# Optimization experiments

Measured on AMD Instinct MI355X. Metric: run time of the kernel, lower is better.

Reference implementation:

```python
import jax, jax.numpy as jnp
import numpy as np

S, B, D, H = 2048, 2, 1024, 16
DK = D // H
SCALE = 1.0 / np.sqrt(DK)


def setup_inputs() -> dict:
    key = jax.random.key(0)
    ks = jax.random.split(key, 8)
    return {
        "query": jax.random.normal(ks[0], (S, B, D), dtype=jnp.float32),
        "key": jax.random.normal(ks[1], (S, B, D), dtype=jnp.float32),
        "value": jax.random.normal(ks[2], (S, B, D), dtype=jnp.float32),
        "mask": jax.random.randint(ks[3], (B, S, S), 0, 2, dtype=jnp.int32),
        "in_proj_weight": jax.random.normal(ks[4], (3 * D, D), dtype=jnp.float32) * 0.02,
        "in_proj_bias": jax.random.normal(ks[5], (3 * D,), dtype=jnp.float32) * 0.02,
        "out_proj_weight": jax.random.normal(ks[6], (D, D), dtype=jnp.float32) * 0.02,
        "out_proj_bias": jax.random.normal(ks[7], (D,), dtype=jnp.float32) * 0.02,
    }


def reference(query, key, value, mask, in_proj_weight, in_proj_bias,
              out_proj_weight, out_proj_bias):
    seq_len, batch, d_model = query.shape
    # split fused in-projection: order is query, key, value
    Wq, Wk, Wv = in_proj_weight[:D], in_proj_weight[D:2 * D], in_proj_weight[2 * D:]
    bq, bk, bv = in_proj_bias[:D], in_proj_bias[D:2 * D], in_proj_bias[2 * D:]
    # PrepareForMultiHeadAttention: x @ W^T + b, then split heads -> [s, b, h, d_k]
    q = (query @ Wq.T + bq).reshape(seq_len, batch, H, DK)
    k = (key @ Wk.T + bk).reshape(key.shape[0], batch, H, DK)
    v = (value @ Wv.T + bv).reshape(value.shape[0], batch, H, DK)
    # scores [i, j, b, h] in float32, scaled
    scores = jnp.einsum('ibhd,jbhd->ijbh', q, k).astype(jnp.float32) * SCALE
    # mask: [b, q, k] -> permute(1,2,0) -> [q, k, b] -> unsqueeze(-1)
    m = jnp.transpose(mask, (1, 2, 0))[..., None]
    scores = jnp.where(m == 1, jnp.float32(-1e9), scores)
    # softmax over key axis (dim=1)
    attn = jax.nn.softmax(scores, axis=1)
    # dropout p=0.0 -> identity
    x = jnp.einsum('ijbh,jbhd->ibhd', attn, v).reshape(seq_len, batch, -1)
    return x @ out_proj_weight.T + out_proj_bias
```

## Files before the change

kernel.cpp:

```cpp
#include <hip/hip_runtime.h>
#include <hip/hip_bf16.h>

typedef unsigned short u16;
typedef unsigned int   u32;
typedef unsigned long long u64;
typedef __bf16 bf16x8 __attribute__((ext_vector_type(8)));
typedef float  f32x4  __attribute__((ext_vector_type(4)));

#define S_LEN  2048
#define BATCH  2
#define DMODEL 1024
#define NHEADS 16
#define DKH    64
#define MWORDS (S_LEN/64)
#define ATT_SCALE 0.125f

__device__ __forceinline__ u16 f2bf(float f){
  u32 x = __builtin_bit_cast(u32, f);
  x += 0x7fffu + ((x >> 16) & 1u);
  return (u16)(x >> 16);
}
__device__ __forceinline__ bf16x8 ld8(const u16* p){ return *(const bf16x8*)p; }

__device__ __forceinline__ void gload16(const u16* g, u16* l){
  __builtin_amdgcn_global_load_lds(
      (const __attribute__((address_space(1))) u32*)(u64)g,
      (__attribute__((address_space(3))) u32*)(u64)l,
      16, 0, 0);
}

__global__ __launch_bounds__(256) void cvt_kernel(
    const float* __restrict__ a0, const float* __restrict__ a1, const float* __restrict__ a2,
    const float* __restrict__ wi, const float* __restrict__ wo, const int* __restrict__ msk,
    u16* __restrict__ d0, u16* __restrict__ d1, u16* __restrict__ d2,
    u16* __restrict__ dwi, u16* __restrict__ dwo, u64* __restrict__ mbits)
{
  int tid = blockIdx.x*256 + threadIdx.x;
  int stride = gridDim.x*256;
  const int NX = S_LEN*BATCH*DMODEL/4;
  for (int i = tid; i < NX; i += stride){
    f32x4 x0 = ((const f32x4*)a0)[i];
    f32x4 x1 = ((const f32x4*)a1)[i];
    f32x4 x2 = ((const f32x4*)a2)[i];
    ((ushort4*)d0)[i] = make_ushort4(f2bf(x0[0]), f2bf(x0[1]), f2bf(x0[2]), f2bf(x0[3]));
    ((ushort4*)d1)[i] = make_ushort4(f2bf(x1[0]), f2bf(x1[1]), f2bf(x1[2]), f2bf(x1[3]));
    ((ushort4*)d2)[i] = make_ushort4(f2bf(x2[0]), f2bf(x2[1]), f2bf(x2[2]), f2bf(x2[3]));
  }
  const int NWI = 3*DMODEL*DMODEL/4;
  for (int i = tid; i < NWI; i += stride){
    f32x4 x = ((const f32x4*)wi)[i];
    ((ushort4*)dwi)[i] = make_ushort4(f2bf(x[0]), f2bf(x[1]), f2bf(x[2]), f2bf(x[3]));
  }
  const int NWO = DMODEL*DMODEL/4;
  for (int i = tid; i < NWO; i += stride){
    f32x4 x = ((const f32x4*)wo)[i];
    ((ushort4*)dwo)[i] = make_ushort4(f2bf(x[0]), f2bf(x[1]), f2bf(x[2]), f2bf(x[3]));
  }
  int gw   = tid >> 6;
  int lane = threadIdx.x & 63;
  int nwaves = stride >> 6;
  const int NW = BATCH*S_LEN*MWORDS;
  for (int w4 = gw*4; w4 < NW; w4 += nwaves*4){
    int v0 = msk[(size_t)(w4+0)*64 + lane];
    int v1 = msk[(size_t)(w4+1)*64 + lane];
    int v2 = msk[(size_t)(w4+2)*64 + lane];
    int v3 = msk[(size_t)(w4+3)*64 + lane];
    u64 b0 = __ballot(v0 != 0);
    u64 b1 = __ballot(v1 != 0);
    u64 b2 = __ballot(v2 != 0);
    u64 b3 = __ballot(v3 != 0);
    if (lane == 0){
      mbits[w4+0] = b0; mbits[w4+1] = b1;
      mbits[w4+2] = b2; mbits[w4+3] = b3;
    }
  }
}

__device__ __forceinline__ void gemm128_loop(
    const u16* __restrict__ A, const u16* __restrict__ W,
    u16* abuf, u16* bbuf, int tid, f32x4 acc[4][4])
{
  int lane = tid & 63, quad = lane >> 4, r = lane & 15;
  int wv = tid >> 6, wm = (wv & 1)*64, wn = (wv >> 1)*64;
  int c0 = tid, c1 = tid + 256;
  int r0 = c0 >> 2, g0 = ((c0 & 3) ^ (r0 & 3))*8;
  int r1 = c1 >> 2, g1 = ((c1 & 3) ^ (r1 & 3))*8;
  const u16* ga0 = A + (size_t)r0*DMODEL + g0;
  const u16* ga1 = A + (size_t)r1*DMODEL + g1;
  const u16* gb0 = W + (size_t)r0*DMODEL + g0;
  const u16* gb1 = W + (size_t)r1*DMODEL + g1;
  int sw = (quad ^ (r & 3))*8;

  auto stage = [&](int bu, int k0){
    u16* ab = abuf + bu*(128*32);
    u16* bb = bbuf + bu*(128*32);
    gload16(ga0 + k0, ab + c0*8);
    gload16(ga1 + k0, ab + c1*8);
    gload16(gb0 + k0, bb + c0*8);
    gload16(gb1 + k0, bb + c1*8);
  };
  auto step = [&](int bu){
    const u16* ab = abuf + bu*(128*32);
    const u16* bb = bbuf + bu*(128*32);
    bf16x8 af[4], bfr[4];
    #pragma unroll
    for (int i = 0; i < 4; ++i) af[i]  = ld8(&ab[(wm + i*16 + r)*32 + sw]);
    #pragma unroll
    for (int i = 0; i < 4; ++i) bfr[i] = ld8(&bb[(wn + i*16 + r)*32 + sw]);
    #pragma unroll
    for (int mi = 0; mi < 4; ++mi)
      #pragma unroll
      for (int ni = 0; ni < 4; ++ni)
        acc[mi][ni] = __builtin_amdgcn_mfma_f32_16x16x32_bf16(af[mi], bfr[ni], acc[mi][ni], 0,0,0);
  };

  stage(0, 0);
  __syncthreads();
  for (int k0 = 0; k0 < DMODEL; k0 += 64){
    stage(1, k0 + 32);
    step(0);
    __syncthreads();
    if (k0 + 64 < DMODEL) stage(0, k0 + 64);
    step(1);
    __syncthreads();
  }
}

__global__ __launch_bounds__(256) void qkv_proj_kernel(
    const u16* __restrict__ xq, const u16* __restrict__ xk, const u16* __restrict__ xv,
    const u16* __restrict__ w, const float* __restrict__ bias,
    u16* __restrict__ q_ws, u16* __restrict__ k_ws, u16* __restrict__ vt_ws)
{
  __shared__ __align__(16) u16 abuf[2*128*32];
  __shared__ __align__(16) u16 bbuf[2*128*32];
  int tid = threadIdx.x;
  int lane = tid & 63, quad = lane >> 4, r = lane & 15;
  int wv = tid >> 6, wm = (wv & 1)*64, wn = (wv >> 1)*64;
  int m0 = blockIdx.x*128, n0 = blockIdx.y*128;
  int t = n0 >> 10;
  const u16* X = (t == 0) ? xq : (t == 1) ? xk : xv;

  f32x4 acc[4][4] = {};
  gemm128_loop(X + (size_t)m0*DMODEL, w + (size_t)n0*DMODEL, abuf, bbuf, tid, acc);

  int mbase = m0 + wm, nbase = n0 + wn;
  #pragma unroll
  for (int ni = 0; ni < 4; ++ni){
    int n  = nbase + ni*16 + r;
    float bv = bias[n];
    int nn = n & (DMODEL-1);
    int h = nn >> 6, dk = nn & 63;
    #pragma unroll
    for (int mi = 0; mi < 4; ++mi){
      #pragma unroll
      for (int reg = 0; reg < 4; ++reg){
        int m = mbase + mi*16 + quad*4 + reg;
        int s = m >> 1, b = m & 1;
        u16 hv = f2bf(acc[mi][ni][reg] + bv);
        size_t bh = (size_t)(b*NHEADS + h);
        if (t == 0)      q_ws [(bh*S_LEN + s)*DKH + dk] = hv;
        else if (t == 1) k_ws [(bh*S_LEN + s)*DKH + dk] = hv;
        else             vt_ws[(bh*DKH + dk)*S_LEN + s] = hv;
      }
    }
  }
}

__global__ __launch_bounds__(256) void attn_kernel(
    const u16* __restrict__ q_ws, const u16* __restrict__ k_ws, const u16* __restrict__ vt_ws,
    const u64* __restrict__ mbits, u16* __restrict__ x_ws)
{
  __shared__ __align__(16) u16 kbuf[2][64*72];
  __shared__ __align__(16) u16 vbuf[2][64*72];
  __shared__ __align__(16) u16 pbuf[4][16*72];
  int tid  = threadIdx.x;
  int wv   = tid >> 6;
  int lane = tid & 63;
  int quad = lane >> 4, r = lane & 15;

  int lin  = blockIdx.y * 32 + blockIdx.x;
  int xcd  = lin & 7, slot = lin >> 3;
  int bh   = (xcd << 2) | (slot >> 5);
  int xt   = slot & 31;
  int b  = bh >> 4, h = bh & 15;
  int i0 = (xt*4 + wv) * 16;

  const u16* Q  = q_ws  + (size_t)bh*S_LEN*DKH;
  const u16* K  = k_ws  + (size_t)bh*S_LEN*DKH;
  const u16* Vt = vt_ws + (size_t)bh*DKH*S_LEN;
  const u64* MB = mbits + ((size_t)b*S_LEN + (i0 + r))*MWORDS;

  int f1 = tid + 256;
  int sr0 = tid >> 3, sc0 = (tid & 7)*8;
  int sr1 = f1  >> 3, sc1 = (f1  & 7)*8;

  const u16* qrow = Q + (size_t)(i0 + r)*DKH + quad*8;
  bf16x8 qf0 = ld8(qrow), qf1 = ld8(qrow + 32);

  float l_part = 0.f;
  f32x4 o[4] = {};
  f32x4 z = {0.f, 0.f, 0.f, 0.f};
  u16* pl = pbuf[wv];

  bf16x8 ak0, ak1, av0, av1, bk0, bk1, bv0, bv1;

  auto loadset = [&](bf16x8& kv0, bf16x8& kv1, bf16x8& vv0, bf16x8& vv1, int j0){
    kv0 = ld8(K  + (size_t)(j0 + sr0)*DKH + sc0);
    kv1 = ld8(K  + (size_t)(j0 + sr1)*DKH + sc1);
    vv0 = ld8(Vt + (size_t)sr0*S_LEN + j0 + sc0);
    vv1 = ld8(Vt + (size_t)sr1*S_LEN + j0 + sc1);
  };
  auto storeset = [&](u16* kb, u16* vb, bf16x8 kv0, bf16x8 kv1, bf16x8 vv0, bf16x8 vv1){
    *(bf16x8*)&kb[sr0*72 + sc0] = kv0;
    *(bf16x8*)&kb[sr1*72 + sc1] = kv1;
    *(bf16x8*)&vb[sr0*72 + sc0] = vv0;
    *(bf16x8*)&vb[sr1*72 + sc1] = vv1;
  };
  auto compute = [&](const u16* kb, const u16* vb, u64 mb){
    float p[16];
    #pragma unroll
    for (int c = 0; c < 4; ++c){
      bf16x8 ka = ld8(&kb[(16*c + r)*72 + quad*8]);
      bf16x8 k8 = ld8(&kb[(16*c + r)*72 + 32 + quad*8]);
      __builtin_amdgcn_s_setprio(1);
      f32x4 s = __builtin_amdgcn_mfma_f32_16x16x32_bf16(ka, qf0, z, 0,0,0);
      s       = __builtin_amdgcn_mfma_f32_16x16x32_bf16(k8, qf1, s, 0,0,0);
      __builtin_amdgcn_s_setprio(0);
      u32 mc = (u32)(mb >> (16*c + 4*quad));
      p[c*4+0] = (mc & 1u) ? 0.f : __expf(s[0]*ATT_SCALE);
      p[c*4+1] = (mc & 2u) ? 0.f : __expf(s[1]*ATT_SCALE);
      p[c*4+2] = (mc & 4u) ? 0.f : __expf(s[2]*ATT_SCALE);
      p[c*4+3] = (mc & 8u) ? 0.f : __expf(s[3]*ATT_SCALE);
      l_part += p[c*4+0] + p[c*4+1] + p[c*4+2] + p[c*4+3];
    }
    #pragma unroll
    for (int c = 0; c < 4; ++c)
      *(ushort4*)&pl[r*72 + 16*c + quad*4] =
        make_ushort4(f2bf(p[c*4+0]), f2bf(p[c*4+1]), f2bf(p[c*4+2]), f2bf(p[c*4+3]));
    asm volatile("s_waitcnt lgkmcnt(0)" ::: "memory");
    bf16x8 pf0 = ld8(&pl[r*72 + quad*8]);
    bf16x8 pf1 = ld8(&pl[r*72 + 32 + quad*8]);
    __builtin_amdgcn_s_setprio(1);
    #pragma unroll
    for (int tt = 0; tt < 4; ++tt){
      bf16x8 va = ld8(&vb[(tt*16 + r)*72 + quad*8]);
      bf16x8 v8 = ld8(&vb[(tt*16 + r)*72 + 32 + quad*8]);
      o[tt] = __builtin_amdgcn_mfma_f32_16x16x32_bf16(pf0, va, o[tt], 0,0,0);
      o[tt] = __builtin_amdgcn_mfma_f32_16x16x32_bf16(pf1, v8, o[tt], 0,0,0);
    }
    __builtin_amdgcn_s_setprio(0);
  };

  loadset(ak0, ak1, av0, av1, 0);
  storeset(kbuf[0], vbuf[0], ak0, ak1, av0, av1);
  loadset(bk0, bk1, bv0, bv1, 64);
  __syncthreads();

  for (int j0 = 0; j0 < S_LEN; j0 += 128){
    storeset(kbuf[1], vbuf[1], bk0, bk1, bv0, bv1);
    if (j0 + 128 < S_LEN) loadset(ak0, ak1, av0, av1, j0 + 128);
    compute(kbuf[0], vbuf[0], MB[j0 >> 6]);
    __syncthreads();
    if (j0 + 128 < S_LEN) storeset(kbuf[0], vbuf[0], ak0, ak1, av0, av1);
    if (j0 + 192 < S_LEN) loadset(bk0, bk1, bv0, bv1, j0 + 192);
    compute(kbuf[1], vbuf[1], MB[(j0 >> 6) + 1]);
    __syncthreads();
  }

  l_part += __shfl_xor(l_part, 16, 64);
  l_part += __shfl_xor(l_part, 32, 64);
  float l0 = 1.f/__shfl(l_part, quad*4+0, 64);
  float l1 = 1.f/__shfl(l_part, quad*4+1, 64);
  float l2 = 1.f/__shfl(l_part, quad*4+2, 64);
  float l3 = 1.f/__shfl(l_part, quad*4+3, 64);
  #pragma unroll
  for (int tt = 0; tt < 4; ++tt){
    int col = h*DKH + tt*16 + r;
    x_ws[((size_t)(i0 + quad*4 + 0)*BATCH + b)*DMODEL + col] = f2bf(o[tt][0]*l0);
    x_ws[((size_t)(i0 + quad*4 + 1)*BATCH + b)*DMODEL + col] = f2bf(o[tt][1]*l1);
    x_ws[((size_t)(i0 + quad*4 + 2)*BATCH + b)*DMODEL + col] = f2bf(o[tt][2]*l2);
    x_ws[((size_t)(i0 + quad*4 + 3)*BATCH + b)*DMODEL + col] = f2bf(o[tt][3]*l3);
  }
}

__global__ __launch_bounds__(256) void out_proj_kernel(
    const u16* __restrict__ x, const u16* __restrict__ w, const float* __restrict__ bias,
    float* __restrict__ out)
{
  __shared__ __align__(16) u16 abuf[2*128*32];
  __shared__ __align__(16) u16 bbuf[2*128*32];
  int tid = threadIdx.x;
  int lane = tid & 63, quad = lane >> 4, r = lane & 15;
  int wv = tid >> 6, wm = (wv & 1)*64, wn = (wv >> 1)*64;
  int m0 = blockIdx.x*128, n0 = blockIdx.y*128;

  f32x4 acc[4][4] = {};
  gemm128_loop(x + (size_t)m0*DMODEL, w + (size_t)n0*DMODEL, abuf, bbuf, tid, acc);

  int mbase = m0 + wm, nbase = n0 + wn;
  #pragma unroll
  for (int ni = 0; ni < 4; ++ni){
    int n = nbase + ni*16 + r;
    float bv = bias[n];
    #pragma unroll
    for (int mi = 0; mi < 4; ++mi){
      #pragma unroll
      for (int reg = 0; reg < 4; ++reg){
        int m = mbase + mi*16 + quad*4 + reg;
        out[(size_t)m*DMODEL + n] = acc[mi][ni][reg] + bv;
      }
    }
  }
}

extern "C" void kernel_launch(void* const* d_in, const int* in_sizes, int n_in,
                              void* d_out, int out_size, void* d_ws, size_t ws_size,
                              hipStream_t stream) {
  (void)in_sizes; (void)n_in; (void)out_size; (void)ws_size;
  const float* query = (const float*)d_in[0];
  const float* key   = (const float*)d_in[1];
  const float* value = (const float*)d_in[2];
  const int*   mask  = (const int*)d_in[3];
  const float* w_in  = (const float*)d_in[4];
  const float* b_in  = (const float*)d_in[5];
  const float* w_out = (const float*)d_in[6];
  const float* b_out = (const float*)d_in[7];
  float* out = (float*)d_out;

  const size_t TSZ = (size_t)BATCH*NHEADS*S_LEN*DKH;
  const size_t XSZ = (size_t)S_LEN*BATCH*DMODEL;
  u16* q_ws  = (u16*)d_ws;
  u16* k_ws  = q_ws  + TSZ;
  u16* vt_ws = k_ws  + TSZ;
  u16* x_ws  = vt_ws + TSZ;
  u16* xq_bf = x_ws  + XSZ;
  u16* xk_bf = xq_bf + XSZ;
  u16* xv_bf = xk_bf + XSZ;
  u16* wi_bf = xv_bf + XSZ;
  u16* wo_bf = wi_bf + (size_t)3*DMODEL*DMODEL;
  u64* mb_ws = (u64*)(wo_bf + (size_t)DMODEL*DMODEL);

  cvt_kernel<<<1024, 256, 0, stream>>>(query, key, value, w_in, w_out, mask,
                                       xq_bf, xk_bf, xv_bf, wi_bf, wo_bf, mb_ws);
  qkv_proj_kernel<<<dim3(32, 24), 256, 0, stream>>>(xq_bf, xk_bf, xv_bf, wi_bf, b_in,
                                                    q_ws, k_ws, vt_ws);
  attn_kernel<<<dim3(32, 32), 256, 0, stream>>>(q_ws, k_ws, vt_ws, mb_ws, x_ws);
  out_proj_kernel<<<dim3(32, 8), 256, 0, stream>>>(x_ws, wo_bf, b_out, out);
}
```

Before: 289.0 us.

## Double attention block to 8 waves with XOR-swizzled LDS tiles and packed bf16 convert

The attention kernel now uses 512-thread blocks of 8 waves covering 128 query rows, so each K/V tile staged in LDS is shared by twice as many waves and per-thread global loads are halved. The padded 72-stride LDS layout is replaced by a 64-stride XOR swizzle for the K, V and P buffers to avoid bank conflicts without padding. The P conversion uses the packed v_cvt_pk_bf16_f32 instruction. The trade-offs are fewer blocks in the grid, more threads waiting at each barrier, and more swizzle index arithmetic.

New measurement: 251.2 us. 13.1% less time.

```diff
diff --git a/kernel.cpp b/kernel.cpp
--- a/kernel.cpp
+++ b/kernel.cpp
@@ -21,6 +21,12 @@
   return (u16)(x >> 16);
 }
 __device__ __forceinline__ bf16x8 ld8(const u16* p){ return *(const bf16x8*)p; }
+
+__device__ __forceinline__ u32 pk_bf16(float a, float b){
+  u32 d;
+  asm("v_cvt_pk_bf16_f32 %0, %1, %2" : "=v"(d) : "v"(a), "v"(b));
+  return d;
+}
 
 __device__ __forceinline__ void gload16(const u16* g, u16* l){
   __builtin_amdgcn_global_load_lds(
@@ -166,62 +172,67 @@
   }
 }
 
-__global__ __launch_bounds__(256) void attn_kernel(
+__global__ __launch_bounds__(512) void attn_kernel(
     const u16* __restrict__ q_ws, const u16* __restrict__ k_ws, const u16* __restrict__ vt_ws,
     const u64* __restrict__ mbits, u16* __restrict__ x_ws)
 {
-  __shared__ __align__(16) u16 kbuf[2][64*72];
-  __shared__ __align__(16) u16 vbuf[2][64*72];
-  __shared__ __align__(16) u16 pbuf[4][16*72];
+  __shared__ __align__(16) u16 kbuf[2][64*64];
+  __shared__ __align__(16) u16 vbuf[2][64*64];
+  __shared__ __align__(16) u16 pbuf[8][16*64];
   int tid  = threadIdx.x;
   int wv   = tid >> 6;
   int lane = tid & 63;
   int quad = lane >> 4, r = lane & 15;
 
-  int lin  = blockIdx.y * 32 + blockIdx.x;
+  int lin  = blockIdx.y * 16 + blockIdx.x;
   int xcd  = lin & 7, slot = lin >> 3;
-  int bh   = (xcd << 2) | (slot >> 5);
-  int xt   = slot & 31;
+  int bh   = (xcd << 2) | (slot >> 4);
+  int xt   = slot & 15;
   int b  = bh >> 4, h = bh & 15;
-  int i0 = (xt*4 + wv) * 16;
+  int i0 = (xt*8 + wv) * 16;
 
   const u16* Q  = q_ws  + (size_t)bh*S_LEN*DKH;
   const u16* K  = k_ws  + (size_t)bh*S_LEN*DKH;
   const u16* Vt = vt_ws + (size_t)bh*DKH*S_LEN;
   const u64* MB = mbits + ((size_t)b*S_LEN + (i0 + r))*MWORDS;
 
-  int f1 = tid + 256;
-  int sr0 = tid >> 3, sc0 = (tid & 7)*8;
-  int sr1 = f1  >> 3, sc1 = (f1  & 7)*8;
+  int sr  = tid >> 3;
+  int sc8 = (tid & 7) * 8;
+  int ssw = ((tid & 7) ^ (sr & 7)) * 8;
+  const u16* Kp = K  + (size_t)sr*DKH   + sc8;
+  const u16* Vp = Vt + (size_t)sr*S_LEN + sc8;
 
   const u16* qrow = Q + (size_t)(i0 + r)*DKH + quad*8;
   bf16x8 qf0 = ld8(qrow), qf1 = ld8(qrow + 32);
+
+  int m7   = r & 7;
+  int ksw0 = (quad ^ m7) * 8;
+  int ksw1 = ksw0 ^ 32;
+  int pw0  = ((quad >> 1) ^ m7) * 8 + (quad & 1)*4;
 
   float l_part = 0.f;
   f32x4 o[4] = {};
   f32x4 z = {0.f, 0.f, 0.f, 0.f};
   u16* pl = pbuf[wv];
 
-  bf16x8 ak0, ak1, av0, av1, bk0, bk1, bv0, bv1;
-
-  auto loadset = [&](bf16x8& kv0, bf16x8& kv1, bf16x8& vv0, bf16x8& vv1, int j0){
-    kv0 = ld8(K  + (size_t)(j0 + sr0)*DKH + sc0);
-    kv1 = ld8(K  + (size_t)(j0 + sr1)*DKH + sc1);
-    vv0 = ld8(Vt + (size_t)sr0*S_LEN + j0 + sc0);
-    vv1 = ld8(Vt + (size_t)sr1*S_LEN + j0 + sc1);
-  };
-  auto storeset = [&](u16* kb, u16* vb, bf16x8 kv0, bf16x8 kv1, bf16x8 vv0, bf16x8 vv1){
-    *(bf16x8*)&kb[sr0*72 + sc0] = kv0;
-    *(bf16x8*)&kb[sr1*72 + sc1] = kv1;
-    *(bf16x8*)&vb[sr0*72 + sc0] = vv0;
-    *(bf16x8*)&vb[sr1*72 + sc1] = vv1;
-  };
-  auto compute = [&](const u16* kb, const u16* vb, u64 mb){
+  bf16x8 ka_, va_, kb_, vb_;
+  auto loadset = [&](bf16x8& kv, bf16x8& vv, int j0){
+    kv = ld8(Kp + (size_t)j0*DKH);
+    vv = ld8(Vp + j0);
+  };
+  auto storeset = [&](int bu, bf16x8 kv, bf16x8 vv){
+    *(bf16x8*)&kbuf[bu][sr*64 + ssw] = kv;
+    *(bf16x8*)&vbuf[bu][sr*64 + ssw] = vv;
+  };
+  auto compute = [&](int bu, u64 mb){
+    const u16* kb = kbuf[bu];
+    const u16* vb = vbuf[bu];
     float p[16];
     #pragma unroll
     for (int c = 0; c < 4; ++c){
-      bf16x8 ka = ld8(&kb[(16*c + r)*72 + quad*8]);
-      bf16x8 k8 = ld8(&kb[(16*c + r)*72 + 32 + quad*8]);
+      int rowb = (16*c + r)*64;
+      bf16x8 ka = ld8(&kb[rowb + ksw0]);
+      bf16x8 k8 = ld8(&kb[rowb + ksw1]);
       __builtin_amdgcn_s_setprio(1);
       f32x4 s = __builtin_amdgcn_mfma_f32_16x16x32_bf16(ka, qf0, z, 0,0,0);
       s       = __builtin_amdgcn_mfma_f32_16x16x32_bf16(k8, qf1, s, 0,0,0);
@@ -234,36 +245,39 @@
       l_part += p[c*4+0] + p[c*4+1] + p[c*4+2] + p[c*4+3];
     }
     #pragma unroll
-    for (int c = 0; c < 4; ++c)
-      *(ushort4*)&pl[r*72 + 16*c + quad*4] =
-        make_ushort4(f2bf(p[c*4+0]), f2bf(p[c*4+1]), f2bf(p[c*4+2]), f2bf(p[c*4+3]));
+    for (int c = 0; c < 4; ++c){
+      u32 k0 = pk_bf16(p[c*4+0], p[c*4+1]);
+      u32 k1 = pk_bf16(p[c*4+2], p[c*4+3]);
+      *(uint2*)&pl[r*64 + ((pw0 & ~7) ^ (2*c*8)) + (pw0 & 7)] = make_uint2(k0, k1);
+    }
     asm volatile("s_waitcnt lgkmcnt(0)" ::: "memory");
-    bf16x8 pf0 = ld8(&pl[r*72 + quad*8]);
-    bf16x8 pf1 = ld8(&pl[r*72 + 32 + quad*8]);
+    bf16x8 pf0 = ld8(&pl[r*64 + ksw0]);
+    bf16x8 pf1 = ld8(&pl[r*64 + ksw1]);
     __builtin_amdgcn_s_setprio(1);
     #pragma unroll
     for (int tt = 0; tt < 4; ++tt){
-      bf16x8 va = ld8(&vb[(tt*16 + r)*72 + quad*8]);
-      bf16x8 v8 = ld8(&vb[(tt*16 + r)*72 + 32 + quad*8]);
+      int rowb = (tt*16 + r)*64;
+      bf16x8 va = ld8(&vb[rowb + ksw0]);
+      bf16x8 v8 = ld8(&vb[rowb + ksw1]);
       o[tt] = __builtin_amdgcn_mfma_f32_16x16x32_bf16(pf0, va, o[tt], 0,0,0);
       o[tt] = __builtin_amdgcn_mfma_f32_16x16x32_bf16(pf1, v8, o[tt], 0,0,0);
     }
     __builtin_amdgcn_s_setprio(0);
   };
 
-  loadset(ak0, ak1, av0, av1, 0);
-  storeset(kbuf[0], vbuf[0], ak0, ak1, av0, av1);
-  loadset(bk0, bk1, bv0, bv1, 64);
+  loadset(ka_, va_, 0);
+  storeset(0, ka_, va_);
+  loadset(kb_, vb_, 64);
   __syncthreads();
 
   for (int j0 = 0; j0 < S_LEN; j0 += 128){
-    storeset(kbuf[1], vbuf[1], bk0, bk1, bv0, bv1);
-    if (j0 + 128 < S_LEN) loadset(ak0, ak1, av0, av1, j0 + 128);
-    compute(kbuf[0], vbuf[0], MB[j0 >> 6]);
+    storeset(1, kb_, vb_);
+    if (j0 + 128 < S_LEN) loadset(ka_, va_, j0 + 128);
+    compute(0, MB[j0 >> 6]);
     __syncthreads();
-    if (j0 + 128 < S_LEN) storeset(kbuf[0], vbuf[0], ak0, ak1, av0, av1);
-    if (j0 + 192 < S_LEN) loadset(bk0, bk1, bv0, bv1, j0 + 192);
-    compute(kbuf[1], vbuf[1], MB[(j0 >> 6) + 1]);
+    if (j0 + 128 < S_LEN) storeset(0, ka_, va_);
+    if (j0 + 192 < S_LEN) loadset(kb_, vb_, j0 + 192);
+    compute(1, MB[(j0 >> 6) + 1]);
     __syncthreads();
   }
 
@@ -344,6 +358,6 @@
                                        xq_bf, xk_bf, xv_bf, wi_bf, wo_bf, mb_ws);
   qkv_proj_kernel<<<dim3(32, 24), 256, 0, stream>>>(xq_bf, xk_bf, xv_bf, wi_bf, b_in,
                                                     q_ws, k_ws, vt_ws);
-  attn_kernel<<<dim3(32, 32), 256, 0, stream>>>(q_ws, k_ws, vt_ws, mb_ws, x_ws);
+  attn_kernel<<<dim3(16, 32), 512, 0, stream>>>(q_ws, k_ws, vt_ws, mb_ws, x_ws);
   out_proj_kernel<<<dim3(32, 8), 256, 0, stream>>>(x_ws, wo_bf, b_out, out);
 }
```
